# Optimization experiments

Hardware: AMD Instinct MI355X
Metric: run time of the kernel (lower is better)

## Reference

```python
import jax, jax.numpy as jnp
import numpy as np
import math

B, T, C, H, D, R = 1, 2048, 2048, 16, 128, 64
W_LOCAL = 512
DELTA_I = 0.75
ROPE_BASE = 10000.0


def _rotate(x):
    # interleaved rotate-half, exactly as in the torch source
    x1, x2 = x[..., ::2], x[..., 1::2]
    return jnp.stack((-x2, x1), axis=-1).reshape(x.shape)


def _rope_tables(seq_len):
    inv_freq = 1.0 / (ROPE_BASE ** (jnp.arange(0, D, 2, dtype=jnp.float32) / D))
    t = jnp.arange(seq_len, dtype=jnp.float32)
    freqs = jnp.einsum('i,j->ij', t, inv_freq)          # [T, D/2]
    emb = jnp.concatenate((freqs, freqs), axis=-1)      # [T, D] (half-layout, as in source)
    return jnp.cos(emb)[None, None], jnp.sin(emb)[None, None]


def setup_inputs() -> dict:
    key = jax.random.key(0)
    ks = jax.random.split(key, 8)
    s = 0.02
    return {
        'x': jax.random.normal(ks[0], (B, T, C), dtype=jnp.float32),
        'w_qkv': jax.random.normal(ks[1], (3 * C, C), dtype=jnp.float32) * s,
        'w_o': jax.random.normal(ks[2], (C, C), dtype=jnp.float32) * s,
        'pk': jax.random.normal(ks[3], (R, D), dtype=jnp.float32) * s,
        'pv': jax.random.normal(ks[4], (R, D), dtype=jnp.float32) * s,
        'uo': jax.random.normal(ks[5], (D, R), dtype=jnp.float32) * s,
        'info_w1': jax.random.normal(ks[6], (C // 4, C), dtype=jnp.float32) * s,
        'info_w2': jax.random.normal(ks[7], (1, C // 4), dtype=jnp.float32) * s,
    }


def reference(x, w_qkv, w_o, pk, pv, uo, info_w1, info_w2):
    Bx, Tx, Cx = x.shape
    scale = 1.0 / math.sqrt(D)

    qkv = x @ w_qkv.T                                   # [B,T,3C]
    q, k, v = jnp.split(qkv, 3, axis=-1)
    q = q.reshape(Bx, Tx, H, D).transpose(0, 2, 1, 3)   # [B,H,T,D]
    k = k.reshape(Bx, Tx, H, D).transpose(0, 2, 1, 3)
    v = v.reshape(Bx, Tx, H, D).transpose(0, 2, 1, 3)

    cos, sin = _rope_tables(Tx)
    q = q * cos + _rotate(q) * sin
    k = k * cos + _rotate(k) * sin

    # causal local-window attention (full [B,H,T,T] scores, as in source)
    w = min(W_LOCAL, Tx)
    idx = jnp.arange(Tx)
    rel = idx[None, :] - idx[:, None]                   # j - i
    local_mask = (rel > 0) | (rel < -(w - 1))           # True = masked
    scores = jnp.einsum('bhtd,bhsd->bhts', q, k) * scale
    scores = jnp.where(local_mask[None, None], -jnp.inf, scores)
    attn_local = jax.nn.softmax(scores, axis=-1)
    ctx_local = jnp.einsum('bhts,bhsd->bhtd', attn_local, v)

    # informational gate (no-grad path in source)
    h_info = jax.nn.gelu(x @ info_w1.T, approximate=False)
    info_score = jax.nn.sigmoid((h_info @ info_w2.T)[..., 0])   # [B,T]
    gate = (info_score > DELTA_I).astype(x.dtype)

    # low-rank global path (unmasked softmax over all tokens, as in source)
    k_r = jnp.einsum('bhsd,rd->bhsr', k, pk)
    v_r = jnp.einsum('bhsd,rd->bhsr', v, pv)
    q_r = jnp.einsum('bhtd,rd->bhtr', q, pk)
    scores_g = jnp.einsum('bhtr,bhsr->bhts', q_r, k_r) * (scale * D / R)
    attn_g = jax.nn.softmax(scores_g, axis=-1)
    ctx_g_r = jnp.einsum('bhts,bhsr->bhtr', attn_g, v_r)
    ctx_g = jnp.einsum('bhtr,dr->bhtd', ctx_g_r, uo)
    gate_q = gate[:, None, :, None]                     # [B,1,T,1]
    ctx = ctx_local + ctx_g * gate_q

    ctx = ctx.transpose(0, 2, 1, 3).reshape(Bx, Tx, Cx)
    return ctx @ w_o.T
```

## Files before the change

kernel.cpp:

```cpp
#include <hip/hip_runtime.h>
#include <hip/hip_bf16.h>
#include <math.h>

#define T_LEN 2048
#define C_DIM 2048
#define NH 16
#define HD 128
#define RANK 64
#define W_LOCAL 512
#define QKV_LD 6144
#define ROW_BF 12288
#define KB_OFF 4096
#define VB_OFF 8192
#define WO_OFF 6144
#define SCALE 0.08838834764831845f
#define SCALE_G 0.17677669529663687f
#define LOG1E4_OVER_64 0.14391156831212787f

typedef __bf16 bf16_t;
typedef __bf16 bf16x8 __attribute__((ext_vector_type(8)));
typedef __bf16 bf16x4 __attribute__((ext_vector_type(4)));
typedef float f32x4 __attribute__((ext_vector_type(4)));

__device__ __forceinline__ void async_copy16(const bf16_t* g, bf16_t* l) {
    __builtin_amdgcn_global_load_lds(
        (const __attribute__((address_space(1))) unsigned int*)g,
        (__attribute__((address_space(3))) unsigned int*)l, 16, 0, 0);
}

__global__ __launch_bounds__(256)
void prep_kernel(const float* __restrict__ x, bf16_t* __restrict__ xb,
                 bf16_t* __restrict__ xlo,
                 const float* __restrict__ w1, bf16_t* __restrict__ w1hi,
                 bf16_t* __restrict__ w1lo,
                 const float* __restrict__ w_qkv, bf16_t* __restrict__ wqb,
                 float* __restrict__ tab) {
    const int bid = blockIdx.x;
    const int tid = threadIdx.x;
    if (bid < 2560) {
        const float* in;
        bf16_t *hi, *lo;
        int idx;
        if (bid < 2048) { in = x; hi = xb; lo = xlo; idx = bid * 256 + tid; }
        else            { in = w1; hi = w1hi; lo = w1lo; idx = (bid - 2048) * 256 + tid; }
        const float* p = in + (size_t)idx * 8;
        float4 v0 = *(const float4*)p;
        float4 v1 = *(const float4*)(p + 4);
        float v[8] = {v0.x, v0.y, v0.z, v0.w, v1.x, v1.y, v1.z, v1.w};
        bf16x8 h, l;
#pragma unroll
        for (int i = 0; i < 8; ++i) {
            bf16_t hb = (bf16_t)v[i];
            h[i] = hb;
            l[i] = (bf16_t)(v[i] - (float)hb);
        }
        *(bf16x8*)(hi + (size_t)idx * 8) = h;
        *(bf16x8*)(lo + (size_t)idx * 8) = l;
    } else if (bid < 8704) {
        int idx = (bid - 2560) * 256 + tid;
        const float* p = w_qkv + (size_t)idx * 8;
        float4 v0 = *(const float4*)p;
        float4 v1 = *(const float4*)(p + 4);
        bf16x8 o;
        o[0] = (bf16_t)v0.x; o[1] = (bf16_t)v0.y; o[2] = (bf16_t)v0.z; o[3] = (bf16_t)v0.w;
        o[4] = (bf16_t)v1.x; o[5] = (bf16_t)v1.y; o[6] = (bf16_t)v1.z; o[7] = (bf16_t)v1.w;
        *(bf16x8*)(wqb + (size_t)idx * 8) = o;
    } else {
        int idx = (bid - 8704) * 256 + tid;
        int t = idx >> 6, j = idx & 63;
        float inv = expf(-(float)j * LOG1E4_OVER_64);
        float s, c;
        sincosf((float)t * inv, &s, &c);
        tab[t * 128 + j] = c;
        tab[t * 128 + 64 + j] = s;
    }
}

#define NTK 32

#define STG_A(bb, ktile) do {                                                  \
    _Pragma("unroll")                                                          \
    for (int c_ = 0; c_ < 4; ++c_)                                             \
        async_copy16(gA + (size_t)(c_ * 32) * 2048 + (ktile) * 64,             \
                     &lds[bb][0][(c_ * 32 + rS) * 64 + dS]);                   \
} while (0)

#define STG_B(bb, ktile) do {                                                  \
    _Pragma("unroll")                                                          \
    for (int c_ = 0; c_ < 4; ++c_)                                             \
        async_copy16(gB + (size_t)(c_ * 32) * 2048 + (ktile) * 64,             \
                     &lds[bb][1][(c_ * 32 + rS) * 64 + dS]);                   \
} while (0)

#define RD_A(bb, m, k) (*(const bf16x8*)&lds[bb][0][(wr * 64 + (m) * 16 + l16) * 64 + (((k) * 4 + quad) ^ xsw) * 8])
#define RD_B(bb, n, k) (*(const bf16x8*)&lds[bb][1][(wc * 64 + (n) * 16 + l16) * 64 + (((k) * 4 + quad) ^ xsw) * 8])

__global__ __launch_bounds__(256, 2)
void gemm_qkv_rope(const bf16_t* __restrict__ A, const bf16_t* __restrict__ B,
                   bf16_t* __restrict__ qkv_bf, bf16_t* __restrict__ vt,
                   const float* __restrict__ tab, const float* __restrict__ w_o) {
    const int bid = blockIdx.x;
    const int tid = threadIdx.x;
    if (bid >= 768) {
        int row = bid - 768;
        int c = tid * 8;
        const float* p = w_o + (size_t)row * 2048 + c;
        float4 v0 = *(const float4*)p;
        float4 v1 = *(const float4*)(p + 4);
        bf16x8 o;
        o[0] = (bf16_t)v0.x; o[1] = (bf16_t)v0.y; o[2] = (bf16_t)v0.z; o[3] = (bf16_t)v0.w;
        o[4] = (bf16_t)v1.x; o[5] = (bf16_t)v1.y; o[6] = (bf16_t)v1.z; o[7] = (bf16_t)v1.w;
        *(bf16x8*)(qkv_bf + (size_t)row * ROW_BF + WO_OFF + c) = o;
        return;
    }

    __shared__ __align__(16) bf16_t lds[2][2][128 * 64];

    const int xcd = bid & 7, idx = bid >> 3;
    const int bn_ = xcd * 6 + (idx >> 4);
    const int bm_ = idx & 15;
    const int wave = tid >> 6, lane = tid & 63;
    const int quad = lane >> 4, l16 = lane & 15;
    const int wr = wave >> 1, wc = wave & 1;
    const int xsw = l16 & 7;

    const int rS = tid >> 3;
    const int cS = ((tid & 7) ^ (rS & 7)) * 8;
    const int dS = (tid & 7) * 8;
    const bf16_t* gA = A + (size_t)(bm_ * 128 + rS) * 2048 + cS;
    const bf16_t* gB = B + (size_t)(bn_ * 128 + rS) * 2048 + cS;

    f32x4 acc[4][4];
#pragma unroll
    for (int i = 0; i < 4; ++i)
#pragma unroll
        for (int j = 0; j < 4; ++j) acc[i][j] = (f32x4){0.f, 0.f, 0.f, 0.f};

    STG_A(0, 0); STG_B(0, 0);
    STG_A(1, 1); STG_B(1, 1);
    asm volatile("s_waitcnt vmcnt(8)" ::: "memory");
    __builtin_amdgcn_s_barrier();

    for (int kt = 0; kt < NTK; ++kt) {
        const int b = kt & 1;
        bf16x8 af[4][2], bfr[4][2];
#pragma unroll
        for (int m = 0; m < 4; ++m) { af[m][0] = RD_A(b, m, 0); af[m][1] = RD_A(b, m, 1); }
#pragma unroll
        for (int n = 0; n < 4; ++n) { bfr[n][0] = RD_B(b, n, 0); bfr[n][1] = RD_B(b, n, 1); }
        asm volatile("s_waitcnt lgkmcnt(0)" ::: "memory");
        __builtin_amdgcn_s_barrier();

        __builtin_amdgcn_s_setprio(1);
#pragma unroll
        for (int m = 0; m < 4; ++m)
#pragma unroll
            for (int n = 0; n < 4; ++n)
                acc[m][n] = __builtin_amdgcn_mfma_f32_16x16x32_bf16(af[m][0], bfr[n][0], acc[m][n], 0, 0, 0);
        __builtin_amdgcn_s_setprio(0);
        if (kt + 2 < NTK) STG_A(b, kt + 2);

        __builtin_amdgcn_s_setprio(1);
#pragma unroll
        for (int m = 0; m < 4; ++m)
#pragma unroll
            for (int n = 0; n < 4; ++n)
                acc[m][n] = __builtin_amdgcn_mfma_f32_16x16x32_bf16(af[m][1], bfr[n][1], acc[m][n], 0, 0, 0);
        __builtin_amdgcn_s_setprio(0);
        if (kt + 2 < NTK) STG_B(b, kt + 2);

        if (kt < NTK - 2) { asm volatile("s_waitcnt vmcnt(8)" ::: "memory"); }
        else              { asm volatile("s_waitcnt vmcnt(0)" ::: "memory"); }
        __builtin_amdgcn_s_barrier();
    }

    const int colbase = bn_ * 128 + wc * 64;
    const int region = (bn_ * 128) >> 11;
    const int rowbase = bm_ * 128 + wr * 64;
    const bool odd = (l16 & 1);

    if (region == 2) {
#pragma unroll
        for (int mt = 0; mt < 4; ++mt)
#pragma unroll
            for (int r = 0; r < 4; ++r) {
                int t = rowbase + mt * 16 + quad * 4 + r;
                bf16_t* brow = qkv_bf + (size_t)t * ROW_BF + VB_OFF + (colbase - 4096);
#pragma unroll
                for (int nt = 0; nt < 4; ++nt)
                    brow[nt * 16 + l16] = (bf16_t)acc[mt][nt][r];
            }
        bf16_t* Tl = (bf16_t*)lds;
#pragma unroll
        for (int mt = 0; mt < 4; ++mt)
#pragma unroll
            for (int r = 0; r < 4; ++r) {
                int rloc = wr * 64 + mt * 16 + quad * 4 + r;
#pragma unroll
                for (int nt = 0; nt < 4; ++nt) {
                    int cloc = wc * 64 + nt * 16 + l16;
                    Tl[cloc * 136 + rloc] = (bf16_t)acc[mt][nt][r];
                }
            }
        __syncthreads();
        const int hh = bn_ - 32;
        const int d = tid >> 1, th = (tid & 1) * 64;
        bf16_t* dst = vt + ((size_t)(hh * 128 + d)) * 2048 + bm_ * 128 + th;
        const bf16_t* srcT = Tl + d * 136 + th;
#pragma unroll
        for (int j = 0; j < 8; ++j)
            *(bf16x8*)(dst + j * 8) = *(const bf16x8*)(srcT + j * 8);
    } else {
#pragma unroll
        for (int mt = 0; mt < 4; ++mt)
#pragma unroll
            for (int r = 0; r < 4; ++r) {
                int t = rowbase + mt * 16 + quad * 4 + r;
                const float* trow = tab + t * 128;
#pragma unroll
                for (int nt = 0; nt < 4; ++nt) {
                    float v = acc[mt][nt][r];
                    float vp = __shfl_xor(v, 1);
                    int col = colbase + nt * 16 + l16;
                    int j = col & 63;
                    float c = trow[j], s = trow[64 + j];
                    float y = odd ? (v * c + vp * s) : (v * c - vp * s);
                    qkv_bf[(size_t)t * ROW_BF + (region == 0 ? col : col + 2048)] = (bf16_t)y;
                }
            }
    }
}

#define STG_A2(bb, ktile) do {                                                 \
    _Pragma("unroll")                                                          \
    for (int c_ = 0; c_ < 4; ++c_)                                             \
        async_copy16(gA + (size_t)(c_ * 32) * 2048 + (ktile) * 64,             \
                     &lds[bb][0][(c_ * 32 + rS) * 64 + dS]);                   \
} while (0)

#define STG_B2(bb, ktile) do {                                                 \
    _Pragma("unroll")                                                          \
    for (int c_ = 0; c_ < 4; ++c_)                                             \
        async_copy16(gB + (size_t)(c_ * 32) * ROW_BF + (ktile) * 64,           \
                     &lds[bb][1][(c_ * 32 + rS) * 64 + dS]);                   \
} while (0)

__global__ __launch_bounds__(256, 2)
void gemm_ctx_wo(const bf16_t* __restrict__ A, const bf16_t* __restrict__ Bov,
                 float* __restrict__ C) {
    __shared__ __align__(16) bf16_t lds[2][2][128 * 64];

    const int bid = blockIdx.x;
    const int xcd = bid & 7, idx = bid >> 3;
    const int bn_ = xcd * 2 + (idx >> 4);
    const int bm_ = idx & 15;
    const int tid = threadIdx.x;
    const int wave = tid >> 6, lane = tid & 63;
    const int quad = lane >> 4, l16 = lane & 15;
    const int wr = wave >> 1, wc = wave & 1;
    const int xsw = l16 & 7;

    const int rS = tid >> 3;
    const int cS = ((tid & 7) ^ (rS & 7)) * 8;
    const int dS = (tid & 7) * 8;
    const bf16_t* gA = A + (size_t)(bm_ * 128 + rS) * 2048 + cS;
    const bf16_t* gB = Bov + (size_t)(bn_ * 128 + rS) * ROW_BF + cS;

    f32x4 acc[4][4];
#pragma unroll
    for (int i = 0; i < 4; ++i)
#pragma unroll
        for (int j = 0; j < 4; ++j) acc[i][j] = (f32x4){0.f, 0.f, 0.f, 0.f};

    STG_A2(0, 0); STG_B2(0, 0);
    STG_A2(1, 1); STG_B2(1, 1);
    asm volatile("s_waitcnt vmcnt(8)" ::: "memory");
    __builtin_amdgcn_s_barrier();

    for (int kt = 0; kt < NTK; ++kt) {
        const int b = kt & 1;
        bf16x8 af[4][2], bfr[4][2];
#pragma unroll
        for (int m = 0; m < 4; ++m) { af[m][0] = RD_A(b, m, 0); af[m][1] = RD_A(b, m, 1); }
#pragma unroll
        for (int n = 0; n < 4; ++n) { bfr[n][0] = RD_B(b, n, 0); bfr[n][1] = RD_B(b, n, 1); }
        asm volatile("s_waitcnt lgkmcnt(0)" ::: "memory");
        __builtin_amdgcn_s_barrier();

        __builtin_amdgcn_s_setprio(1);
#pragma unroll
        for (int m = 0; m < 4; ++m)
#pragma unroll
            for (int n = 0; n < 4; ++n)
                acc[m][n] = __builtin_amdgcn_mfma_f32_16x16x32_bf16(af[m][0], bfr[n][0], acc[m][n], 0, 0, 0);
        __builtin_amdgcn_s_setprio(0);
        if (kt + 2 < NTK) STG_A2(b, kt + 2);

        __builtin_amdgcn_s_setprio(1);
#pragma unroll
        for (int m = 0; m < 4; ++m)
#pragma unroll
            for (int n = 0; n < 4; ++n)
                acc[m][n] = __builtin_amdgcn_mfma_f32_16x16x32_bf16(af[m][1], bfr[n][1], acc[m][n], 0, 0, 0);
        __builtin_amdgcn_s_setprio(0);
        if (kt + 2 < NTK) STG_B2(b, kt + 2);

        if (kt < NTK - 2) { asm volatile("s_waitcnt vmcnt(8)" ::: "memory"); }
        else              { asm volatile("s_waitcnt vmcnt(0)" ::: "memory"); }
        __builtin_amdgcn_s_barrier();
    }

    const int colbase = bn_ * 128 + wc * 64;
    const int rowbase = bm_ * 128 + wr * 64;
#pragma unroll
    for (int mt = 0; mt < 4; ++mt)
#pragma unroll
        for (int r = 0; r < 4; ++r) {
            int row = rowbase + mt * 16 + quad * 4 + r;
            float* crow = C + (size_t)row * 2048 + colbase;
#pragma unroll
            for (int nt = 0; nt < 4; ++nt)
                crow[nt * 16 + l16] = acc[mt][nt][r];
        }
}

#define GBK 32

__global__ __launch_bounds__(256)
void info_gemm_mfma(const bf16_t* __restrict__ Ahi, const bf16_t* __restrict__ Alo,
                    const bf16_t* __restrict__ Bhi, const bf16_t* __restrict__ Blo,
                    float* __restrict__ Cpart) {
    __shared__ bf16_t Ah[128 * GBK];
    __shared__ bf16_t Al[128 * GBK];
    __shared__ bf16_t Bh[128 * GBK];
    __shared__ bf16_t Bl[128 * GBK];
    const int tid = threadIdx.x;
    const int wave = tid >> 6, lane = tid & 63;
    const int quad = lane >> 4, l16 = lane & 15;
    const int bm = blockIdx.y * 128, bn = blockIdx.x * 128;
    const int ks = blockIdx.z;
    const int wm = (wave >> 1) * 64, wn = (wave & 1) * 64;
    const int lrow = lane >> 2;
    const int lkb = (lane & 3) * 8;
    const int kbeg = ks * 512;

    f32x4 acc[4][4];
#pragma unroll
    for (int i = 0; i < 4; ++i)
#pragma unroll
        for (int j = 0; j < 4; ++j) acc[i][j] = (f32x4){0.f, 0.f, 0.f, 0.f};

    const size_t aoff = (size_t)(bm + wave * 16 + lrow) * 2048 + lkb + kbeg;
    const size_t boff = (size_t)(bn + wave * 16 + lrow) * 2048 + lkb + kbeg;
    bf16_t* lAh = &Ah[(wave * 16 + lrow) * GBK + lkb];
    bf16_t* lAl = &Al[(wave * 16 + lrow) * GBK + lkb];
    bf16_t* lBh = &Bh[(wave * 16 + lrow) * GBK + lkb];
    bf16_t* lBl = &Bl[(wave * 16 + lrow) * GBK + lkb];

    for (int k0 = 0; k0 < 512; k0 += GBK) {
        __syncthreads();
        async_copy16(Ahi + aoff + k0, lAh);
        async_copy16(Ahi + aoff + (size_t)64 * 2048 + k0, lAh + 64 * GBK);
        async_copy16(Alo + aoff + k0, lAl);
        async_copy16(Alo + aoff + (size_t)64 * 2048 + k0, lAl + 64 * GBK);
        async_copy16(Bhi + boff + k0, lBh);
        async_copy16(Bhi + boff + (size_t)64 * 2048 + k0, lBh + 64 * GBK);
        async_copy16(Blo + boff + k0, lBl);
        async_copy16(Blo + boff + (size_t)64 * 2048 + k0, lBl + 64 * GBK);
        __syncthreads();

        bf16x8 ah[4], al[4], bh[4], bl[4];
#pragma unroll
        for (int mt = 0; mt < 4; ++mt) {
            ah[mt] = *(const bf16x8*)&Ah[(wm + mt * 16 + l16) * GBK + quad * 8];
            al[mt] = *(const bf16x8*)&Al[(wm + mt * 16 + l16) * GBK + quad * 8];
        }
#pragma unroll
        for (int nt = 0; nt < 4; ++nt) {
            bh[nt] = *(const bf16x8*)&Bh[(wn + nt * 16 + l16) * GBK + quad * 8];
            bl[nt] = *(const bf16x8*)&Bl[(wn + nt * 16 + l16) * GBK + quad * 8];
        }
#pragma unroll
        for (int mt = 0; mt < 4; ++mt)
#pragma unroll
            for (int nt = 0; nt < 4; ++nt) {
                acc[mt][nt] = __builtin_amdgcn_mfma_f32_16x16x32_bf16(ah[mt], bh[nt], acc[mt][nt], 0, 0, 0);
                acc[mt][nt] = __builtin_amdgcn_mfma_f32_16x16x32_bf16(ah[mt], bl[nt], acc[mt][nt], 0, 0, 0);
                acc[mt][nt] = __builtin_amdgcn_mfma_f32_16x16x32_bf16(al[mt], bh[nt], acc[mt][nt], 0, 0, 0);
            }
    }

    float* cp = Cpart + (size_t)ks * 2048 * 512;
#pragma unroll
    for (int mt = 0; mt < 4; ++mt)
#pragma unroll
        for (int r = 0; r < 4; ++r) {
            int row = bm + wm + mt * 16 + quad * 4 + r;
            float* crow = cp + (size_t)row * 512 + bn + wn;
#pragma unroll
            for (int nt = 0; nt < 4; ++nt)
                crow[nt * 16 + l16] = acc[mt][nt][r];
        }
}

__device__ __forceinline__ float gelu_exact(float v) {
    return 0.5f * v * (1.0f + erff(v * 0.70710678118654752f));
}

__global__ __launch_bounds__(64)
void info_gate_kernel(const float* __restrict__ Cpart, const float* __restrict__ w2,
                      float* __restrict__ gate) {
    const int t = blockIdx.x;
    const int lane = threadIdx.x;
    const float* p0 = Cpart + (size_t)t * 512;
    float s = 0.f;
#pragma unroll
    for (int i = lane; i < 512; i += 64) {
        float v = ((p0[i] + p0[i + 1048576]) + p0[i + 2097152]) + p0[i + 3145728];
        s += gelu_exact(v) * w2[i];
    }
#pragma unroll
    for (int off = 32; off > 0; off >>= 1) s += __shfl_down(s, off);
    if (lane == 0) {
        float sig = 1.f / (1.f + expf(-s));
        gate[t] = (sig > 0.75f) ? 1.f : 0.f;
    }
}

#define KV_LD 136

__global__ __launch_bounds__(256)
void kvr_mfma_kernel(const bf16_t* __restrict__ qkv_bf,
                     const float* __restrict__ pk, const float* __restrict__ pv,
                     float* __restrict__ kr, float* __restrict__ vr,
                     bf16_t* __restrict__ qr) {
    __shared__ bf16_t Kt[64 * KV_LD];
    __shared__ bf16_t Vt[64 * KV_LD];
    __shared__ bf16_t Qt[64 * KV_LD];
    __shared__ bf16_t Pk[64 * KV_LD];
    __shared__ bf16_t Pv[64 * KV_LD];

    const int h = blockIdx.y;
    const int s0 = blockIdx.x * 64;
    const int tid = threadIdx.x;
    const int wave = tid >> 6, lane = tid & 63;
    const int quad = lane >> 4, l16 = lane & 15;

#pragma unroll
    for (int i = 0; i < 4; ++i) {
        int gid = i * 256 + tid;
        int row = gid >> 4, ch = (gid & 15) << 3;
        const bf16_t* rb = qkv_bf + (size_t)(s0 + row) * ROW_BF + h * HD + ch;
        *(bf16x8*)&Qt[row * KV_LD + ch] = *(const bf16x8*)(rb);
        *(bf16x8*)&Kt[row * KV_LD + ch] = *(const bf16x8*)(rb + KB_OFF);
        *(bf16x8*)&Vt[row * KV_LD + ch] = *(const bf16x8*)(rb + VB_OFF);
    }
#pragma unroll
    for (int i = 0; i < 8; ++i) {
        int gid = i * 256 + tid;
        int row = gid >> 5, c = (gid & 31) << 2;
        float4 wk = *(const float4*)(pk + (size_t)row * HD + c);
        float4 wv = *(const float4*)(pv + (size_t)row * HD + c);
        bf16x4 qk4, qv4;
        qk4[0] = (bf16_t)wk.x; qk4[1] = (bf16_t)wk.y; qk4[2] = (bf16_t)wk.z; qk4[3] = (bf16_t)wk.w;
        qv4[0] = (bf16_t)wv.x; qv4[1] = (bf16_t)wv.y; qv4[2] = (bf16_t)wv.z; qv4[3] = (bf16_t)wv.w;
        *(bf16x4*)&Pk[row * KV_LD + c] = qk4;
        *(bf16x4*)&Pv[row * KV_LD + c] = qv4;
    }
    __syncthreads();

    f32x4 ak[4], av[4], aq[4];
#pragma unroll
    for (int nt = 0; nt < 4; ++nt) {
        ak[nt] = (f32x4){0.f, 0.f, 0.f, 0.f};
        av[nt] = (f32x4){0.f, 0.f, 0.f, 0.f};
        aq[nt] = (f32x4){0.f, 0.f, 0.f, 0.f};
    }

#pragma unroll
    for (int ks = 0; ks < 4; ++ks) {
        const int ao = (wave * 16 + l16) * KV_LD + ks * 32 + quad * 8;
        bf16x8 a_k = *(const bf16x8*)&Kt[ao];
        bf16x8 a_v = *(const bf16x8*)&Vt[ao];
        bf16x8 a_q = *(const bf16x8*)&Qt[ao];
#pragma unroll
        for (int nt = 0; nt < 4; ++nt) {
            const int bo = (nt * 16 + l16) * KV_LD + ks * 32 + quad * 8;
            bf16x8 bk = *(const bf16x8*)&Pk[bo];
            bf16x8 bv = *(const bf16x8*)&Pv[bo];
            ak[nt] = __builtin_amdgcn_mfma_f32_16x16x32_bf16(a_k, bk, ak[nt], 0, 0, 0);
            av[nt] = __builtin_amdgcn_mfma_f32_16x16x32_bf16(a_v, bv, av[nt], 0, 0, 0);
            aq[nt] = __builtin_amdgcn_mfma_f32_16x16x32_bf16(a_q, bk, aq[nt], 0, 0, 0);
        }
    }

#pragma unroll
    for (int nt = 0; nt < 4; ++nt)
#pragma unroll
        for (int r = 0; r < 4; ++r) {
            int s = s0 + wave * 16 + quad * 4 + r;
            size_t idx = ((size_t)h * T_LEN + s) * RANK + nt * 16 + l16;
            kr[idx] = ak[nt][r];
            vr[idx] = av[nt][r];
            qr[idx] = (bf16_t)aq[nt][r];
        }
}

#define QTI 64
#define KTI 64
#define PS_LD 72

__global__ __launch_bounds__(256)
void local_attn_kernel(const bf16_t* __restrict__ qkv_bf, const bf16_t* __restrict__ vt,
                       bf16_t* __restrict__ cxb) {
    __shared__ __align__(16) bf16_t Qs[QTI * 128];
    __shared__ __align__(16) bf16_t Ks[KTI * 128];
    __shared__ __align__(16) bf16_t Vts[128 * KTI];
    __shared__ bf16_t Ps[4][16 * PS_LD];

    const int h = blockIdx.y;
    const int t0 = blockIdx.x * QTI;
    const int tid = threadIdx.x;
    const int wave = tid >> 6, lane = tid & 63;
    const int quad = lane >> 4, l16 = lane & 15;
    const int xsw = l16 & 7;

    const bf16_t* vth = vt + (size_t)h * 128 * 2048;

#pragma unroll
    for (int i = 0; i < 4; ++i) {
        int c = i * 256 + tid;
        int row = c >> 4, pc = c & 15;
        int lc = pc ^ (row & 7);
        async_copy16(qkv_bf + (size_t)(t0 + row) * ROW_BF + h * HD + lc * 8, &Qs[c * 8]);
    }

    f32x4 o[8];
#pragma unroll
    for (int d8 = 0; d8 < 8; ++d8) o[d8] = (f32x4){0.f, 0.f, 0.f, 0.f};
    float m_i[4] = {-1e30f, -1e30f, -1e30f, -1e30f};
    float l_i[4] = {0.f, 0.f, 0.f, 0.f};

    __syncthreads();

    for (int kt = 0; kt < 9; ++kt) {
        const int sbase = t0 - 512 + kt * KTI;
        if (sbase < 0) continue;
        __syncthreads();
#pragma unroll
        for (int i = 0; i < 4; ++i) {
            int c = i * 256 + tid;
            int row = c >> 4, pc = c & 15;
            int lc = pc ^ (row & 7);
            async_copy16(qkv_bf + (size_t)(sbase + row) * ROW_BF + KB_OFF + h * HD + lc * 8,
                         &Ks[c * 8]);
        }
#pragma unroll
        for (int i = 0; i < 4; ++i) {
            int c = i * 256 + tid;
            int row = c >> 3, pc = c & 7;
            int lc = pc ^ (row & 7);
            async_copy16(vth + (size_t)row * 2048 + sbase + lc * 8, &Vts[c * 8]);
        }
        __syncthreads();

        f32x4 sacc[4];
#pragma unroll
        for (int nt = 0; nt < 4; ++nt) sacc[nt] = (f32x4){0.f, 0.f, 0.f, 0.f};
#pragma unroll
        for (int ks = 0; ks < 4; ++ks) {
            bf16x8 a = *(const bf16x8*)&Qs[(wave * 16 + l16) * 128 + (((ks * 4 + quad) ^ xsw)) * 8];
#pragma unroll
            for (int nt = 0; nt < 4; ++nt) {
                bf16x8 b = *(const bf16x8*)&Ks[(nt * 16 + l16) * 128 + (((ks * 4 + quad) ^ xsw)) * 8];
                sacc[nt] = __builtin_amdgcn_mfma_f32_16x16x32_bf16(a, b, sacc[nt], 0, 0, 0);
            }
        }

#pragma unroll
        for (int nt = 0; nt < 4; ++nt)
#pragma unroll
            for (int r = 0; r < 4; ++r) sacc[nt][r] *= SCALE;

        if (kt == 0 || kt == 8) {
#pragma unroll
            for (int nt = 0; nt < 4; ++nt) {
                int s_g = sbase + nt * 16 + l16;
#pragma unroll
                for (int r = 0; r < 4; ++r) {
                    int t_g = t0 + wave * 16 + quad * 4 + r;
                    bool valid = (s_g <= t_g) && (s_g + W_LOCAL > t_g);
                    if (!valid) sacc[nt][r] = -1e30f;
                }
            }
        }

#pragma unroll
        for (int r = 0; r < 4; ++r) {
            float mx = fmaxf(fmaxf(sacc[0][r], sacc[1][r]), fmaxf(sacc[2][r], sacc[3][r]));
            mx = fmaxf(mx, __shfl_xor(mx, 1));
            mx = fmaxf(mx, __shfl_xor(mx, 2));
            mx = fmaxf(mx, __shfl_xor(mx, 4));
            mx = fmaxf(mx, __shfl_xor(mx, 8));
            float mnew = fmaxf(m_i[r], mx);
            float alpha = __expf(m_i[r] - mnew);
            m_i[r] = mnew;
            float rs = 0.f;
#pragma unroll
            for (int nt = 0; nt < 4; ++nt) {
                float p = __expf(sacc[nt][r] - mnew);
                sacc[nt][r] = p;
                rs += p;
            }
            rs += __shfl_xor(rs, 1);
            rs += __shfl_xor(rs, 2);
            rs += __shfl_xor(rs, 4);
            rs += __shfl_xor(rs, 8);
            l_i[r] = l_i[r] * alpha + rs;
#pragma unroll
            for (int d8 = 0; d8 < 8; ++d8) o[d8][r] *= alpha;
        }

#pragma unroll
        for (int r = 0; r < 4; ++r)
#pragma unroll
            for (int nt = 0; nt < 4; ++nt)
                Ps[wave][(quad * 4 + r) * PS_LD + nt * 16 + l16] = (bf16_t)sacc[nt][r];

#pragma unroll
        for (int ks2 = 0; ks2 < 2; ++ks2) {
            bf16x8 a = *(const bf16x8*)&Ps[wave][l16 * PS_LD + ks2 * 32 + quad * 8];
#pragma unroll
            for (int d8 = 0; d8 < 8; ++d8) {
                int rw = d8 * 16 + l16;
                bf16x8 b = *(const bf16x8*)&Vts[rw * 64 + (((ks2 * 4 + quad) ^ xsw)) * 8];
                o[d8] = __builtin_amdgcn_mfma_f32_16x16x32_bf16(a, b, o[d8], 0, 0, 0);
            }
        }
    }

#pragma unroll
    for (int r = 0; r < 4; ++r) {
        float inv = 1.0f / l_i[r];
        size_t rowoff = (size_t)(t0 + wave * 16 + quad * 4 + r) * 2048 + h * HD;
#pragma unroll
        for (int d8 = 0; d8 < 8; ++d8)
            cxb[rowoff + d8 * 16 + l16] = (bf16_t)(o[d8][r] * inv);
    }
}

__device__ __forceinline__ float block_reduce_max512(float v, float* red, int tid) {
    red[tid] = v; __syncthreads();
    for (int s = 256; s > 0; s >>= 1) {
        if (tid < s) red[tid] = fmaxf(red[tid], red[tid + s]);
        __syncthreads();
    }
    float r = red[0]; __syncthreads();
    return r;
}
__device__ __forceinline__ float block_reduce_sum512(float v, float* red, int tid) {
    red[tid] = v; __syncthreads();
    for (int s = 256; s > 0; s >>= 1) {
        if (tid < s) red[tid] = red[tid] + red[tid + s];
        __syncthreads();
    }
    float r = red[0]; __syncthreads();
    return r;
}

__global__ __launch_bounds__(512)
void global_attn_kernel(bf16_t* __restrict__ cxb, const float* __restrict__ kr,
                        const float* __restrict__ vr, const bf16_t* __restrict__ qr,
                        const float* __restrict__ uo, const float* __restrict__ gate) {
    const int t = blockIdx.x, h = blockIdx.y;
    if (gate[t] <= 0.5f) return;

    __shared__ float qrs[64];
    __shared__ float red[512];
    __shared__ float cgr[64];
    __shared__ float sg[2048];
    const int tid = threadIdx.x;

    if (tid < 64) qrs[tid] = (float)qr[((size_t)h * T_LEN + t) * RANK + tid];
    __syncthreads();

    const float* krh = kr + (size_t)h * T_LEN * RANK;
    const float* vrh = vr + (size_t)h * T_LEN * RANK;
    float lmax = -INFINITY;
    for (int s = tid; s < T_LEN; s += 512) {
        const float* krr = krh + (size_t)s * RANK;
        float acc = 0.f;
#pragma unroll
        for (int r = 0; r < RANK; r += 4) {
            float4 k4 = *(const float4*)(krr + r);
            acc += qrs[r] * k4.x + qrs[r + 1] * k4.y + qrs[r + 2] * k4.z + qrs[r + 3] * k4.w;
        }
        float sc = acc * SCALE_G;
        sg[s] = sc;
        lmax = fmaxf(lmax, sc);
    }
    float gmx = block_reduce_max512(lmax, red, tid);
    float lsum = 0.f;
    for (int s = tid; s < T_LEN; s += 512) {
        float pp = expf(sg[s] - gmx);
        sg[s] = pp;
        lsum += pp;
    }
    float gsum = block_reduce_sum512(lsum, red, tid);

    {
        const int r = tid & 63, part = tid >> 6;
        float pacc = 0.f;
        for (int s = part; s < T_LEN; s += 8) pacc += sg[s] * vrh[(size_t)s * RANK + r];
        red[tid] = pacc;
        __syncthreads();
        if (tid < 64) {
            float c = 0.f;
#pragma unroll
            for (int pp = 0; pp < 8; ++pp) c += red[pp * 64 + tid];
            cgr[tid] = c / gsum;
        }
        __syncthreads();
    }

    if (tid < 128) {
        float cg = 0.f;
#pragma unroll
        for (int r = 0; r < RANK; ++r) cg += cgr[r] * uo[tid * RANK + r];
        size_t off = (size_t)t * 2048 + h * HD + tid;
        cxb[off] = (bf16_t)((float)cxb[off] + cg);
    }
}

extern "C" void kernel_launch(void* const* d_in, const int* in_sizes, int n_in,
                              void* d_out, int out_size, void* d_ws, size_t ws_size,
                              hipStream_t stream) {
    const float* x     = (const float*)d_in[0];
    const float* w_qkv = (const float*)d_in[1];
    const float* w_o   = (const float*)d_in[2];
    const float* pk    = (const float*)d_in[3];
    const float* pv    = (const float*)d_in[4];
    const float* uo    = (const float*)d_in[5];
    const float* w1    = (const float*)d_in[6];
    const float* w2    = (const float*)d_in[7];
    float* out = (float*)d_out;

    float* ws = (float*)d_ws;
    float* qkv   = ws;
    float* hinfo = qkv + (size_t)12582912;
    float* gatep = hinfo + (size_t)1048576;
    bf16_t* xb   = (bf16_t*)(gatep + 2048);
    float* wqbf  = gatep + 2048 + 2097152;
    bf16_t* wqb  = (bf16_t*)wqbf;
    float* krp   = wqbf;
    float* vrp   = wqbf + (size_t)2097152;
    float* tabp  = hinfo;
    bf16_t* qrp  = (bf16_t*)hinfo;
    bf16_t* cxb  = xb;
    bf16_t* qkvb = (bf16_t*)qkv;
    bf16_t* wob  = qkvb + WO_OFF;
    bf16_t* vtp  = (bf16_t*)d_out;
    float* ipart  = qkv;
    bf16_t* xlo   = (bf16_t*)(qkv + 4194304);
    bf16_t* w1hi  = (bf16_t*)(qkv + 6291456);
    bf16_t* w1lo  = (bf16_t*)(qkv + 6815744);

    prep_kernel<<<9216, 256, 0, stream>>>(x, xb, xlo, w1, w1hi, w1lo, w_qkv, wqb, tabp);
    info_gemm_mfma<<<dim3(4, 16, 4), 256, 0, stream>>>(xb, xlo, w1hi, w1lo, ipart);
    info_gate_kernel<<<T_LEN, 64, 0, stream>>>(ipart, w2, gatep);
    gemm_qkv_rope<<<2816, 256, 0, stream>>>(xb, wqb, qkvb, vtp, tabp, w_o);
    kvr_mfma_kernel<<<dim3(T_LEN / 64, NH), 256, 0, stream>>>(qkvb, pk, pv, krp, vrp, qrp);
    local_attn_kernel<<<dim3(T_LEN / QTI, NH), 256, 0, stream>>>(qkvb, vtp, cxb);
    global_attn_kernel<<<dim3(T_LEN, NH), 512, 0, stream>>>(cxb, krp, vrp, qrp, uo, gatep);
    gemm_ctx_wo<<<256, 256, 0, stream>>>(cxb, wob, out);
}
```

Before: 307.7 us.

## Fuse info-gate split-bf16 GEMM into QKV GEMM launch, converting fp32 inline

Removes the separate info_gemm_mfma launch and the prep pass that wrote hi/lo bf16 copies of x and info_w1. 128 extra blocks in the QKV GEMM launch now load fp32 x and w1 directly, split them into hi/lo bf16 in registers, and run the 3-MFMA compensated product. The split-K factor drops from 4 to 2, so each block covers a 1024-long K range. This saves a launch and the intermediate hi/lo traffic, and lets the info GEMM overlap with the QKV GEMM. The cost is a synchronous, unpipelined load-convert loop in those blocks, which may become a long tail, and ipart is now placed in the out buffer past vt.

```diff
diff --git a/kernel.cpp b/kernel.cpp
--- a/kernel.cpp
+++ b/kernel.cpp
@@ -30,34 +30,21 @@
 
 __global__ __launch_bounds__(256)
 void prep_kernel(const float* __restrict__ x, bf16_t* __restrict__ xb,
-                 bf16_t* __restrict__ xlo,
-                 const float* __restrict__ w1, bf16_t* __restrict__ w1hi,
-                 bf16_t* __restrict__ w1lo,
                  const float* __restrict__ w_qkv, bf16_t* __restrict__ wqb,
                  float* __restrict__ tab) {
     const int bid = blockIdx.x;
     const int tid = threadIdx.x;
-    if (bid < 2560) {
-        const float* in;
-        bf16_t *hi, *lo;
-        int idx;
-        if (bid < 2048) { in = x; hi = xb; lo = xlo; idx = bid * 256 + tid; }
-        else            { in = w1; hi = w1hi; lo = w1lo; idx = (bid - 2048) * 256 + tid; }
-        const float* p = in + (size_t)idx * 8;
+    if (bid < 2048) {
+        int idx = bid * 256 + tid;
+        const float* p = x + (size_t)idx * 8;
         float4 v0 = *(const float4*)p;
         float4 v1 = *(const float4*)(p + 4);
-        float v[8] = {v0.x, v0.y, v0.z, v0.w, v1.x, v1.y, v1.z, v1.w};
-        bf16x8 h, l;
-#pragma unroll
-        for (int i = 0; i < 8; ++i) {
-            bf16_t hb = (bf16_t)v[i];
-            h[i] = hb;
-            l[i] = (bf16_t)(v[i] - (float)hb);
-        }
-        *(bf16x8*)(hi + (size_t)idx * 8) = h;
-        *(bf16x8*)(lo + (size_t)idx * 8) = l;
-    } else if (bid < 8704) {
-        int idx = (bid - 2560) * 256 + tid;
+        bf16x8 o;
+        o[0] = (bf16_t)v0.x; o[1] = (bf16_t)v0.y; o[2] = (bf16_t)v0.z; o[3] = (bf16_t)v0.w;
+        o[4] = (bf16_t)v1.x; o[5] = (bf16_t)v1.y; o[6] = (bf16_t)v1.z; o[7] = (bf16_t)v1.w;
+        *(bf16x8*)(xb + (size_t)idx * 8) = o;
+    } else if (bid < 8192) {
+        int idx = (bid - 2048) * 256 + tid;
         const float* p = w_qkv + (size_t)idx * 8;
         float4 v0 = *(const float4*)p;
         float4 v1 = *(const float4*)(p + 4);
@@ -66,7 +53,7 @@
         o[4] = (bf16_t)v1.x; o[5] = (bf16_t)v1.y; o[6] = (bf16_t)v1.z; o[7] = (bf16_t)v1.w;
         *(bf16x8*)(wqb + (size_t)idx * 8) = o;
     } else {
-        int idx = (bid - 8704) * 256 + tid;
+        int idx = (bid - 8192) * 256 + tid;
         int t = idx >> 6, j = idx & 63;
         float inv = expf(-(float)j * LOG1E4_OVER_64);
         float s, c;
@@ -77,6 +64,7 @@
 }
 
 #define NTK 32
+#define ILD 40
 
 #define STG_A(bb, ktile) do {                                                  \
     _Pragma("unroll")                                                          \
@@ -98,11 +86,103 @@
 __global__ __launch_bounds__(256, 2)
 void gemm_qkv_rope(const bf16_t* __restrict__ A, const bf16_t* __restrict__ B,
                    bf16_t* __restrict__ qkv_bf, bf16_t* __restrict__ vt,
-                   const float* __restrict__ tab, const float* __restrict__ w_o) {
+                   const float* __restrict__ tab, const float* __restrict__ w_o,
+                   const float* __restrict__ x, const float* __restrict__ w1,
+                   float* __restrict__ ipart) {
+    __shared__ __align__(16) unsigned char smem[65536];
     const int bid = blockIdx.x;
     const int tid = threadIdx.x;
-    if (bid >= 768) {
-        int row = bid - 768;
+
+    if (bid < 128) {
+        bf16_t* Ah = (bf16_t*)smem;
+        bf16_t* Al = Ah + 128 * ILD;
+        bf16_t* Bh = Al + 128 * ILD;
+        bf16_t* Bl = Bh + 128 * ILD;
+        const int bn = bid & 3, bm = (bid >> 2) & 15, ks = bid >> 6;
+        const int wave = tid >> 6, lane = tid & 63;
+        const int quad = lane >> 4, l16 = lane & 15;
+        const int wm = (wave >> 1) * 64, wn = (wave & 1) * 64;
+        const int lrow = lane >> 2;
+        const int lkb = (lane & 3) * 8;
+        const int kbeg = ks * 1024;
+
+        f32x4 acc[4][4];
+#pragma unroll
+        for (int i = 0; i < 4; ++i)
+#pragma unroll
+            for (int j = 0; j < 4; ++j) acc[i][j] = (f32x4){0.f, 0.f, 0.f, 0.f};
+
+        const float* gx = x + (size_t)(bm * 128 + wave * 16 + lrow) * 2048 + kbeg + lkb;
+        const float* gw = w1 + (size_t)(bn * 128 + wave * 16 + lrow) * 2048 + kbeg + lkb;
+        const int wrow = (wave * 16 + lrow) * ILD + lkb;
+
+        for (int k0 = 0; k0 < 1024; k0 += 32) {
+            __syncthreads();
+#pragma unroll
+            for (int hr = 0; hr < 2; ++hr) {
+                const float* px = gx + (size_t)hr * 64 * 2048 + k0;
+                float4 a0 = *(const float4*)px, a1 = *(const float4*)(px + 4);
+                float av[8] = {a0.x, a0.y, a0.z, a0.w, a1.x, a1.y, a1.z, a1.w};
+                bf16x8 h, l;
+#pragma unroll
+                for (int i = 0; i < 8; ++i) {
+                    bf16_t hb = (bf16_t)av[i];
+                    h[i] = hb; l[i] = (bf16_t)(av[i] - (float)hb);
+                }
+                *(bf16x8*)&Ah[wrow + hr * 64 * ILD] = h;
+                *(bf16x8*)&Al[wrow + hr * 64 * ILD] = l;
+
+                const float* pw = gw + (size_t)hr * 64 * 2048 + k0;
+                float4 b0 = *(const float4*)pw, b1 = *(const float4*)(pw + 4);
+                float bv[8] = {b0.x, b0.y, b0.z, b0.w, b1.x, b1.y, b1.z, b1.w};
+                bf16x8 hb2, lb2;
+#pragma unroll
+                for (int i = 0; i < 8; ++i) {
+                    bf16_t hh = (bf16_t)bv[i];
+                    hb2[i] = hh; lb2[i] = (bf16_t)(bv[i] - (float)hh);
+                }
+                *(bf16x8*)&Bh[wrow + hr * 64 * ILD] = hb2;
+                *(bf16x8*)&Bl[wrow + hr * 64 * ILD] = lb2;
+            }
+            __syncthreads();
+
+            bf16x8 ah[4], al[4], bh[4], bl[4];
+#pragma unroll
+            for (int mt = 0; mt < 4; ++mt) {
+                ah[mt] = *(const bf16x8*)&Ah[(wm + mt * 16 + l16) * ILD + quad * 8];
+                al[mt] = *(const bf16x8*)&Al[(wm + mt * 16 + l16) * ILD + quad * 8];
+            }
+#pragma unroll
+            for (int nt = 0; nt < 4; ++nt) {
+                bh[nt] = *(const bf16x8*)&Bh[(wn + nt * 16 + l16) * ILD + quad * 8];
+                bl[nt] = *(const bf16x8*)&Bl[(wn + nt * 16 + l16) * ILD + quad * 8];
+            }
+#pragma unroll
+            for (int mt = 0; mt < 4; ++mt)
+#pragma unroll
+                for (int nt = 0; nt < 4; ++nt) {
+                    acc[mt][nt] = __builtin_amdgcn_mfma_f32_16x16x32_bf16(ah[mt], bh[nt], acc[mt][nt], 0, 0, 0);
+                    acc[mt][nt] = __builtin_amdgcn_mfma_f32_16x16x32_bf16(ah[mt], bl[nt], acc[mt][nt], 0, 0, 0);
+                    acc[mt][nt] = __builtin_amdgcn_mfma_f32_16x16x32_bf16(al[mt], bh[nt], acc[mt][nt], 0, 0, 0);
+                }
+        }
+
+        float* cp = ipart + (size_t)ks * 2048 * 512;
+#pragma unroll
+        for (int mt = 0; mt < 4; ++mt)
+#pragma unroll
+            for (int r = 0; r < 4; ++r) {
+                int row = bm * 128 + wm + mt * 16 + quad * 4 + r;
+                float* crow = cp + (size_t)row * 512 + bn * 128 + wn;
+#pragma unroll
+                for (int nt = 0; nt < 4; ++nt)
+                    crow[nt * 16 + l16] = acc[mt][nt][r];
+            }
+        return;
+    }
+
+    if (bid >= 896) {
+        int row = bid - 896;
         int c = tid * 8;
         const float* p = w_o + (size_t)row * 2048 + c;
         float4 v0 = *(const float4*)p;
@@ -114,9 +194,11 @@
         return;
     }
 
-    __shared__ __align__(16) bf16_t lds[2][2][128 * 64];
-
-    const int xcd = bid & 7, idx = bid >> 3;
+    typedef bf16_t ldsbuf_t[2][128 * 64];
+    ldsbuf_t* lds = (ldsbuf_t*)smem;
+
+    const int gid = bid - 128;
+    const int xcd = gid & 7, idx = gid >> 3;
     const int bn_ = xcd * 6 + (idx >> 4);
     const int bm_ = idx & 15;
     const int wave = tid >> 6, lane = tid & 63;
@@ -190,7 +272,7 @@
                 for (int nt = 0; nt < 4; ++nt)
                     brow[nt * 16 + l16] = (bf16_t)acc[mt][nt][r];
             }
-        bf16_t* Tl = (bf16_t*)lds;
+        bf16_t* Tl = (bf16_t*)smem;
 #pragma unroll
         for (int mt = 0; mt < 4; ++mt)
 #pragma unroll
@@ -248,7 +330,9 @@
 __global__ __launch_bounds__(256, 2)
 void gemm_ctx_wo(const bf16_t* __restrict__ A, const bf16_t* __restrict__ Bov,
                  float* __restrict__ C) {
-    __shared__ __align__(16) bf16_t lds[2][2][128 * 64];
+    __shared__ __align__(16) bf16_t ldss[2][2][128 * 64];
+    typedef bf16_t ldsbuf_t[2][128 * 64];
+    ldsbuf_t* lds = (ldsbuf_t*)ldss;
 
     const int bid = blockIdx.x;
     const int xcd = bid & 7, idx = bid >> 3;
@@ -324,85 +408,6 @@
         }
 }
 
-#define GBK 32
-
-__global__ __launch_bounds__(256)
-void info_gemm_mfma(const bf16_t* __restrict__ Ahi, const bf16_t* __restrict__ Alo,
-                    const bf16_t* __restrict__ Bhi, const bf16_t* __restrict__ Blo,
-                    float* __restrict__ Cpart) {
-    __shared__ bf16_t Ah[128 * GBK];
-    __shared__ bf16_t Al[128 * GBK];
-    __shared__ bf16_t Bh[128 * GBK];
-    __shared__ bf16_t Bl[128 * GBK];
-    const int tid = threadIdx.x;
-    const int wave = tid >> 6, lane = tid & 63;
-    const int quad = lane >> 4, l16 = lane & 15;
-    const int bm = blockIdx.y * 128, bn = blockIdx.x * 128;
-    const int ks = blockIdx.z;
-    const int wm = (wave >> 1) * 64, wn = (wave & 1) * 64;
-    const int lrow = lane >> 2;
-    const int lkb = (lane & 3) * 8;
-    const int kbeg = ks * 512;
-
-    f32x4 acc[4][4];
-#pragma unroll
-    for (int i = 0; i < 4; ++i)
-#pragma unroll
-        for (int j = 0; j < 4; ++j) acc[i][j] = (f32x4){0.f, 0.f, 0.f, 0.f};
-
-    const size_t aoff = (size_t)(bm + wave * 16 + lrow) * 2048 + lkb + kbeg;
-    const size_t boff = (size_t)(bn + wave * 16 + lrow) * 2048 + lkb + kbeg;
-    bf16_t* lAh = &Ah[(wave * 16 + lrow) * GBK + lkb];
-    bf16_t* lAl = &Al[(wave * 16 + lrow) * GBK + lkb];
-    bf16_t* lBh = &Bh[(wave * 16 + lrow) * GBK + lkb];
-    bf16_t* lBl = &Bl[(wave * 16 + lrow) * GBK + lkb];
-
-    for (int k0 = 0; k0 < 512; k0 += GBK) {
-        __syncthreads();
-        async_copy16(Ahi + aoff + k0, lAh);
-        async_copy16(Ahi + aoff + (size_t)64 * 2048 + k0, lAh + 64 * GBK);
-        async_copy16(Alo + aoff + k0, lAl);
-        async_copy16(Alo + aoff + (size_t)64 * 2048 + k0, lAl + 64 * GBK);
-        async_copy16(Bhi + boff + k0, lBh);
-        async_copy16(Bhi + boff + (size_t)64 * 2048 + k0, lBh + 64 * GBK);
-        async_copy16(Blo + boff + k0, lBl);
-        async_copy16(Blo + boff + (size_t)64 * 2048 + k0, lBl + 64 * GBK);
-        __syncthreads();
-
-        bf16x8 ah[4], al[4], bh[4], bl[4];
-#pragma unroll
-        for (int mt = 0; mt < 4; ++mt) {
-            ah[mt] = *(const bf16x8*)&Ah[(wm + mt * 16 + l16) * GBK + quad * 8];
-            al[mt] = *(const bf16x8*)&Al[(wm + mt * 16 + l16) * GBK + quad * 8];
-        }
-#pragma unroll
-        for (int nt = 0; nt < 4; ++nt) {
-            bh[nt] = *(const bf16x8*)&Bh[(wn + nt * 16 + l16) * GBK + quad * 8];
-            bl[nt] = *(const bf16x8*)&Bl[(wn + nt * 16 + l16) * GBK + quad * 8];
-        }
-#pragma unroll
-        for (int mt = 0; mt < 4; ++mt)
-#pragma unroll
-            for (int nt = 0; nt < 4; ++nt) {
-                acc[mt][nt] = __builtin_amdgcn_mfma_f32_16x16x32_bf16(ah[mt], bh[nt], acc[mt][nt], 0, 0, 0);
-                acc[mt][nt] = __builtin_amdgcn_mfma_f32_16x16x32_bf16(ah[mt], bl[nt], acc[mt][nt], 0, 0, 0);
-                acc[mt][nt] = __builtin_amdgcn_mfma_f32_16x16x32_bf16(al[mt], bh[nt], acc[mt][nt], 0, 0, 0);
-            }
-    }
-
-    float* cp = Cpart + (size_t)ks * 2048 * 512;
-#pragma unroll
-    for (int mt = 0; mt < 4; ++mt)
-#pragma unroll
-        for (int r = 0; r < 4; ++r) {
-            int row = bm + wm + mt * 16 + quad * 4 + r;
-            float* crow = cp + (size_t)row * 512 + bn + wn;
-#pragma unroll
-            for (int nt = 0; nt < 4; ++nt)
-                crow[nt * 16 + l16] = acc[mt][nt][r];
-        }
-}
-
 __device__ __forceinline__ float gelu_exact(float v) {
     return 0.5f * v * (1.0f + erff(v * 0.70710678118654752f));
 }
@@ -416,7 +421,7 @@
     float s = 0.f;
 #pragma unroll
     for (int i = lane; i < 512; i += 64) {
-        float v = ((p0[i] + p0[i + 1048576]) + p0[i + 2097152]) + p0[i + 3145728];
+        float v = p0[i] + p0[i + 1048576];
         s += gelu_exact(v) * w2[i];
     }
 #pragma unroll
@@ -760,15 +765,11 @@
     bf16_t* qkvb = (bf16_t*)qkv;
     bf16_t* wob  = qkvb + WO_OFF;
     bf16_t* vtp  = (bf16_t*)d_out;
-    float* ipart  = qkv;
-    bf16_t* xlo   = (bf16_t*)(qkv + 4194304);
-    bf16_t* w1hi  = (bf16_t*)(qkv + 6291456);
-    bf16_t* w1lo  = (bf16_t*)(qkv + 6815744);
-
-    prep_kernel<<<9216, 256, 0, stream>>>(x, xb, xlo, w1, w1hi, w1lo, w_qkv, wqb, tabp);
-    info_gemm_mfma<<<dim3(4, 16, 4), 256, 0, stream>>>(xb, xlo, w1hi, w1lo, ipart);
+    float* ipart = (float*)(vtp + (size_t)16 * 128 * 2048);
+
+    prep_kernel<<<8704, 256, 0, stream>>>(x, xb, w_qkv, wqb, tabp);
+    gemm_qkv_rope<<<2944, 256, 0, stream>>>(xb, wqb, qkvb, vtp, tabp, w_o, x, w1, ipart);
     info_gate_kernel<<<T_LEN, 64, 0, stream>>>(ipart, w2, gatep);
-    gemm_qkv_rope<<<2816, 256, 0, stream>>>(xb, wqb, qkvb, vtp, tabp, w_o);
     kvr_mfma_kernel<<<dim3(T_LEN / 64, NH), 256, 0, stream>>>(qkvb, pk, pv, krp, vrp, qrp);
     local_attn_kernel<<<dim3(T_LEN / QTI, NH), 256, 0, stream>>>(qkvb, vtp, cxb);
     global_attn_kernel<<<dim3(T_LEN, NH), 512, 0, stream>>>(cxb, krp, vrp, qrp, uo, gatep);
```

Result: faster. 294.0 us (-4.5%).
